# Optimization experiments

Measured on AMD Instinct MI355X. Metric: run time of the kernel, lower is better.

## Reference

```python
import jax, jax.numpy as jnp
import numpy as np

D = 768           # input_dim == slot_dim
H, DH = 8, 64     # encoder attention heads / head dim (x-transformers defaults)
INNER = 4 * D     # ff_mult=4 GLU inner dim
EPS = 1e-8
N_ITERS = 3
SCALE = D ** -0.5


def _ln(x, g, b):
    m = jnp.mean(x, axis=-1, keepdims=True)
    v = jnp.var(x, axis=-1, keepdims=True)
    return (x - m) / jnp.sqrt(v + 1e-5) * g + b


def setup_inputs() -> dict:
    key = jax.random.key(0)
    ks = jax.random.split(key, 16)
    w = lambda i, shape, s=0.02: jax.random.normal(ks[i], shape, jnp.float32) * s
    return dict(
        x=jax.random.normal(ks[0], (32, 1024, D), jnp.float32),
        noise=jax.random.normal(ks[1], (32, 16, D), jnp.float32),
        init_mu=jax.random.normal(ks[2], (D,), jnp.float32),
        init_log_sigma=w(3, (D,), 0.05),
        Wk=w(4, (D, D)), Wv=w(5, (D, D)), Wq=w(6, (D, D)),
        ni_g=jnp.ones(D), ni_b=jnp.zeros(D),       # norm_input
        ns_g=jnp.ones(D), ns_b=jnp.zeros(D),       # norm_slots
        nica_g=jnp.ones(D), nica_b=jnp.zeros(D),   # norm_ica
        ln1_g=jnp.ones(D), ln1_b=jnp.zeros(D),     # encoder attn pre-norm
        Wq_a=w(7, (D, H * DH)), Wk_a=w(8, (D, H * DH)),
        Wv_a=w(9, (D, H * DH)), Wo_a=w(10, (H * DH, D)),
        ln2_g=jnp.ones(D), ln2_b=jnp.zeros(D),     # encoder ff pre-norm
        W1=w(11, (D, 2 * INNER)), W2=w(12, (INNER, D)),
        lnf_g=jnp.ones(D), lnf_b=jnp.zeros(D),     # encoder final norm
    )


def _inv_cross_attn(q, k, v):
    # softmax over the SLOT axis (dim i), then renormalize over keys j
    dots = jnp.einsum('bid,bjd->bij', q, k) * SCALE
    attn = jax.nn.softmax(dots, axis=1) + EPS
    attn = attn / jnp.sum(attn, axis=-1, keepdims=True)
    updates = jnp.einsum('bjd,bij->bid', v, attn)
    return updates, attn


def _encoder(h, ln1_g, ln1_b, Wq_a, Wk_a, Wv_a, Wo_a, ln2_g, ln2_b, W1, W2, lnf_g, lnf_b):
    b, n, _ = h.shape
    a = _ln(h, ln1_g, ln1_b)
    q = (a @ Wq_a).reshape(b, n, H, DH)
    k = (a @ Wk_a).reshape(b, n, H, DH)
    v = (a @ Wv_a).reshape(b, n, H, DH)
    scores = jnp.einsum('bihd,bjhd->bhij', q, k) * (DH ** -0.5)
    p = jax.nn.softmax(scores, axis=-1)
    o = jnp.einsum('bhij,bjhd->bihd', p, v).reshape(b, n, H * DH)
    h = h + o @ Wo_a
    f = _ln(h, ln2_g, ln2_b)
    u, g = jnp.split(f @ W1, 2, axis=-1)
    h = h + (u * jax.nn.silu(g)) @ W2
    return _ln(h, lnf_g, lnf_b)


def reference(x, noise, init_mu, init_log_sigma, Wk, Wv, Wq,
              ni_g, ni_b, ns_g, ns_b, nica_g, nica_b,
              ln1_g, ln1_b, Wq_a, Wk_a, Wv_a, Wo_a,
              ln2_g, ln2_b, W1, W2, lnf_g, lnf_b):
    xn = _ln(x, ni_g, ni_b)
    k = xn @ Wk
    v = xn @ Wv
    slots = init_mu + jnp.exp(init_log_sigma) * noise  # [b, n_slots, d]

    def step(slots):
        q = _ln(slots, ns_g, ns_b) @ Wq
        updates, attn = _inv_cross_attn(q, k, v)
        slots = _ln(slots + updates, nica_g, nica_b)
        slots = _encoder(slots, ln1_g, ln1_b, Wq_a, Wk_a, Wv_a, Wo_a,
                         ln2_g, ln2_b, W1, W2, lnf_g, lnf_b)
        return slots, attn

    for _ in range(N_ITERS):
        slots, _ = step(slots)
    slots, attn = step(slots)
    attn_map = jnp.transpose(attn, (0, 2, 1))  # b n hw -> b hw n
    return slots, attn_map
```

## Files before the change

### kernel.cpp

```cpp
#include <hip/hip_runtime.h>
#include <hip/hip_bf16.h>
#include <stdint.h>

typedef _Float16 f16;
typedef __attribute__((ext_vector_type(8))) _Float16 f16x8;
typedef __attribute__((ext_vector_type(4))) _Float16 f16x4;
typedef __attribute__((ext_vector_type(4))) float f32x4;

#define GLOBAL_AS __attribute__((address_space(1)))
#define LDS_AS __attribute__((address_space(3)))

#define D_DIM 768
#define NTOK 1024
#define NSLOT 16
#define NB 32
#define NTOT (NB*NTOK)
#define HDIM 512
#define INNER 3072
#define SCALE_D 0.03608439182435161f
#define SCALE_H 0.125f

template<int OUT>
__global__ __launch_bounds__(256) void mgemm64_k(
    const f16* __restrict__ A, const f16* __restrict__ Bt,
    void* __restrict__ Cout, int M, int N, int K, int Kc)
{
  __shared__ __align__(16) f16 As[64*128];
  __shared__ __align__(16) f16 Bs[64*128];
  const int tid = threadIdx.x;
  const int lane = tid & 63;
  const int wave = tid >> 6;
  const int m0 = blockIdx.x*64, n0 = blockIdx.y*64;
  const int kbeg = blockIdx.z * Kc;
  const int wm = (wave>>1)*32, wn = (wave&1)*32;
  const int quad = lane>>4, l16 = lane&15;

  const int sr = tid>>2;
  const int sc = (tid&3)*8;
  const f16* gA = A  + (size_t)(m0+sr)*K + kbeg + sc;
  const f16* gB = Bt + (size_t)(n0+sr)*K + kbeg + sc;
  LDS_AS f16* lA = (LDS_AS f16*)&As[(size_t)tid*8];
  LDS_AS f16* lB = (LDS_AS f16*)&Bs[(size_t)tid*8];

  const f16* fA0 = &As[(wm + l16)*32 + quad*8];
  const f16* fB0 = &Bs[(wn + l16)*32 + quad*8];

  f32x4 acc[2][2] = {};

  for (int k0 = 0; k0 < Kc; k0 += 128){
    #pragma unroll
    for (int p=0;p<4;++p){
      __builtin_amdgcn_global_load_lds((const GLOBAL_AS void*)(gA + k0 + p*32),
                                       (LDS_AS void*)(lA + (size_t)p*2048), 16, 0, 0);
      __builtin_amdgcn_global_load_lds((const GLOBAL_AS void*)(gB + k0 + p*32),
                                       (LDS_AS void*)(lB + (size_t)p*2048), 16, 0, 0);
    }
    __syncthreads();
    #pragma unroll
    for (int p=0;p<4;++p){
      f16x8 a0 = *(const f16x8*)(fA0 + p*2048);
      f16x8 a1 = *(const f16x8*)(fA0 + p*2048 + 16*32);
      f16x8 b0 = *(const f16x8*)(fB0 + p*2048);
      f16x8 b1 = *(const f16x8*)(fB0 + p*2048 + 16*32);
      acc[0][0] = __builtin_amdgcn_mfma_f32_16x16x32_f16(a0,b0,acc[0][0],0,0,0);
      acc[0][1] = __builtin_amdgcn_mfma_f32_16x16x32_f16(a0,b1,acc[0][1],0,0,0);
      acc[1][0] = __builtin_amdgcn_mfma_f32_16x16x32_f16(a1,b0,acc[1][0],0,0,0);
      acc[1][1] = __builtin_amdgcn_mfma_f32_16x16x32_f16(a1,b1,acc[1][1],0,0,0);
    }
    __syncthreads();
  }
  #pragma unroll
  for (int mt=0;mt<2;++mt){
    #pragma unroll
    for (int nt=0;nt<2;++nt){
      int gm = m0 + wm + mt*16 + quad*4;
      int gn = n0 + wn + nt*16 + l16;
      #pragma unroll
      for (int r=0;r<4;++r){
        float c = acc[mt][nt][r];
        size_t idx = (size_t)(gm+r)*N + gn;
        if (OUT==1) ((f16*)Cout)[idx] = (f16)c;
        else        atomicAdd(&((float*)Cout)[idx], c);
      }
    }
  }
}

__global__ __launch_bounds__(256) void w1glu_k(
    const f16* __restrict__ A, const f16* __restrict__ W1T,
    f16* __restrict__ act, int M)
{
  __shared__ __align__(16) f16 As[64*128];
  __shared__ __align__(16) f16 Bu[64*128];
  __shared__ __align__(16) f16 Bg[64*128];
  const int K = 768;
  const int tid = threadIdx.x;
  const int lane = tid & 63;
  const int wave = tid >> 6;
  const int m0 = blockIdx.x*64, n0 = blockIdx.y*64;
  const int wm = (wave>>1)*32, wn = (wave&1)*32;
  const int quad = lane>>4, l16 = lane&15;

  const int sr = tid>>2;
  const int sc = (tid&3)*8;
  const f16* gA  = A   + (size_t)(m0+sr)*K + sc;
  const f16* gBu = W1T + (size_t)(n0+sr)*K + sc;
  const f16* gBg = W1T + (size_t)(3072+n0+sr)*K + sc;
  LDS_AS f16* lA  = (LDS_AS f16*)&As[(size_t)tid*8];
  LDS_AS f16* lBu = (LDS_AS f16*)&Bu[(size_t)tid*8];
  LDS_AS f16* lBg = (LDS_AS f16*)&Bg[(size_t)tid*8];

  const f16* fA0 = &As[(wm + l16)*32 + quad*8];
  const f16* fU0 = &Bu[(wn + l16)*32 + quad*8];
  const f16* fG0 = &Bg[(wn + l16)*32 + quad*8];

  f32x4 accU[2][2] = {};
  f32x4 accG[2][2] = {};

  for (int k0 = 0; k0 < K; k0 += 128){
    #pragma unroll
    for (int p=0;p<4;++p){
      __builtin_amdgcn_global_load_lds((const GLOBAL_AS void*)(gA  + k0 + p*32),
                                       (LDS_AS void*)(lA  + (size_t)p*2048), 16, 0, 0);
      __builtin_amdgcn_global_load_lds((const GLOBAL_AS void*)(gBu + k0 + p*32),
                                       (LDS_AS void*)(lBu + (size_t)p*2048), 16, 0, 0);
      __builtin_amdgcn_global_load_lds((const GLOBAL_AS void*)(gBg + k0 + p*32),
                                       (LDS_AS void*)(lBg + (size_t)p*2048), 16, 0, 0);
    }
    __syncthreads();
    #pragma unroll
    for (int p=0;p<4;++p){
      f16x8 a0 = *(const f16x8*)(fA0 + p*2048);
      f16x8 a1 = *(const f16x8*)(fA0 + p*2048 + 16*32);
      f16x8 u0 = *(const f16x8*)(fU0 + p*2048);
      f16x8 u1 = *(const f16x8*)(fU0 + p*2048 + 16*32);
      f16x8 g0 = *(const f16x8*)(fG0 + p*2048);
      f16x8 g1 = *(const f16x8*)(fG0 + p*2048 + 16*32);
      accU[0][0] = __builtin_amdgcn_mfma_f32_16x16x32_f16(a0,u0,accU[0][0],0,0,0);
      accU[0][1] = __builtin_amdgcn_mfma_f32_16x16x32_f16(a0,u1,accU[0][1],0,0,0);
      accU[1][0] = __builtin_amdgcn_mfma_f32_16x16x32_f16(a1,u0,accU[1][0],0,0,0);
      accU[1][1] = __builtin_amdgcn_mfma_f32_16x16x32_f16(a1,u1,accU[1][1],0,0,0);
      accG[0][0] = __builtin_amdgcn_mfma_f32_16x16x32_f16(a0,g0,accG[0][0],0,0,0);
      accG[0][1] = __builtin_amdgcn_mfma_f32_16x16x32_f16(a0,g1,accG[0][1],0,0,0);
      accG[1][0] = __builtin_amdgcn_mfma_f32_16x16x32_f16(a1,g0,accG[1][0],0,0,0);
      accG[1][1] = __builtin_amdgcn_mfma_f32_16x16x32_f16(a1,g1,accG[1][1],0,0,0);
    }
    __syncthreads();
  }
  #pragma unroll
  for (int mt=0;mt<2;++mt){
    #pragma unroll
    for (int nt=0;nt<2;++nt){
      int gm = m0 + wm + mt*16 + quad*4;
      int gn = n0 + wn + nt*16 + l16;
      #pragma unroll
      for (int r=0;r<4;++r){
        float u = accU[mt][nt][r];
        float g = accG[mt][nt][r];
        float sg = g / (1.0f + __expf(-g));
        act[(size_t)(gm+r)*INNER + gn] = (f16)(u*sg);
      }
    }
  }
}

__global__ __launch_bounds__(256) void dots_k(
    const f16* __restrict__ Q,
    const f16* __restrict__ Xn,
    f16* __restrict__ attn,
    float* __restrict__ rsPart)
{
  __shared__ __align__(16) f16 qf[16*768];
  __shared__ __align__(16) f16 ks[64*128];
  __shared__ float rpart[4][16];
  const int b = blockIdx.x, jt = blockIdx.y;
  const int tid = threadIdx.x;
  const int lane = tid & 63;
  const int w = tid >> 6;
  const int quad = lane>>4, l16 = lane&15;

  #pragma unroll
  for (int c=0;c<6;++c){
    int p = c*256 + tid;
    int ki = p >> 6, qd = (p >> 4) & 3, rw = p & 15;
    f16x8 v = *(const f16x8*)(Q + ((size_t)(b*NSLOT+rw))*D_DIM + ki*32 + qd*8);
    *(f16x8*)&qf[(size_t)p*8] = v;
  }

  const f16* gK = Xn + ((size_t)(b*NTOK + jt*64 + (tid>>2)))*D_DIM + (tid&3)*8;
  LDS_AS f16* lK = (LDS_AS f16*)&ks[(size_t)tid*8];

  f32x4 acc = {};
  for (int it=0; it<6; ++it){
    #pragma unroll
    for (int p=0;p<4;++p)
      __builtin_amdgcn_global_load_lds((const GLOBAL_AS void*)(gK + it*128 + p*32),
                                       (LDS_AS void*)(lK + (size_t)p*2048), 16, 0, 0);
    __syncthreads();
    #pragma unroll
    for (int p=0;p<4;++p){
      f16x8 a  = *(const f16x8*)&qf[(((size_t)(it*4+p)*4 + quad)*16 + l16)*8];
      f16x8 bf = *(const f16x8*)&ks[(size_t)p*2048 + (w*16+l16)*32 + quad*8];
      acc = __builtin_amdgcn_mfma_f32_16x16x32_f16(a, bf, acc, 0, 0, 0);
    }
    __syncthreads();
  }

  float v0 = acc[0]*SCALE_D, v1 = acc[1]*SCALE_D, v2 = acc[2]*SCALE_D, v3 = acc[3]*SCALE_D;
  float mx = fmaxf(fmaxf(v0,v1), fmaxf(v2,v3));
  mx = fmaxf(mx, __shfl_xor(mx, 16));
  mx = fmaxf(mx, __shfl_xor(mx, 32));
  float e0 = __expf(v0-mx), e1 = __expf(v1-mx), e2 = __expf(v2-mx), e3 = __expf(v3-mx);
  float s = e0+e1+e2+e3;
  s += __shfl_xor(s, 16);
  s += __shfl_xor(s, 32);
  float inv = 1.0f/s;
  float a0 = e0*inv + 1e-8f, a1 = e1*inv + 1e-8f, a2 = e2*inv + 1e-8f, a3 = e3*inv + 1e-8f;

  int jcol = jt*64 + w*16 + l16;
  int ibase = b*NSLOT + quad*4;
  attn[(size_t)(ibase+0)*NTOK + jcol] = (f16)a0;
  attn[(size_t)(ibase+1)*NTOK + jcol] = (f16)a1;
  attn[(size_t)(ibase+2)*NTOK + jcol] = (f16)a2;
  attn[(size_t)(ibase+3)*NTOK + jcol] = (f16)a3;

  float t0=a0, t1=a1, t2=a2, t3=a3;
  #pragma unroll
  for (int m=1;m<16;m<<=1){
    t0 += __shfl_xor(t0, m);
    t1 += __shfl_xor(t1, m);
    t2 += __shfl_xor(t2, m);
    t3 += __shfl_xor(t3, m);
  }
  if (l16 == 0){
    rpart[w][quad*4+0] = t0;
    rpart[w][quad*4+1] = t1;
    rpart[w][quad*4+2] = t2;
    rpart[w][quad*4+3] = t3;
  }
  __syncthreads();
  if (tid < 16){
    float ss = rpart[0][tid] + rpart[1][tid] + rpart[2][tid] + rpart[3][tid];
    rsPart[(size_t)((b*16 + jt)<<4) + tid] = ss;
  }
}

__global__ __launch_bounds__(256) void attnv_k(
    const f16* __restrict__ attn,
    const float* __restrict__ rsPart,
    const f16* __restrict__ XnT,
    const f16* __restrict__ WvT,
    float* __restrict__ accb)
{
  __shared__ __align__(16) f16 Asl[16*128];
  __shared__ __align__(16) f16 Bsl[64*128];
  __shared__ float rsum[16];
  __shared__ __align__(16) f16 tl[16][80];
  const int b = blockIdx.x, d0 = blockIdx.y*64;
  const int tid = threadIdx.x;
  const int lane = tid & 63;
  const int w = tid >> 6;
  const int quad = lane>>4, l16 = lane&15;

  if (tid < 16){
    float s = 0.f;
    #pragma unroll
    for (int jt=0;jt<16;++jt) s += rsPart[(size_t)((b*16 + jt)<<4) + tid];
    rsum[tid] = s;
  }

  const int pa = tid>>6, ta = tid&63;
  const f16* gA = attn + ((size_t)(b*NSLOT + (ta>>2)))*NTOK + pa*32 + (ta&3)*8;
  LDS_AS f16* lA = (LDS_AS f16*)&Asl[(size_t)pa*512 + ta*8];
  const f16* gB = XnT + ((size_t)(d0 + (tid>>2)))*NTOT + b*NTOK + (tid&3)*8;
  LDS_AS f16* lB = (LDS_AS f16*)&Bsl[(size_t)tid*8];

  f32x4 acc = {};
  for (int it=0; it<8; ++it){
    __builtin_amdgcn_global_load_lds((const GLOBAL_AS void*)(gA + it*128),
                                     (LDS_AS void*)lA, 16, 0, 0);
    #pragma unroll
    for (int p=0;p<4;++p)
      __builtin_amdgcn_global_load_lds((const GLOBAL_AS void*)(gB + it*128 + p*32),
                                       (LDS_AS void*)(lB + (size_t)p*2048), 16, 0, 0);
    __syncthreads();
    #pragma unroll
    for (int p=0;p<4;++p){
      f16x8 a  = *(const f16x8*)&Asl[(size_t)p*512 + l16*32 + quad*8];
      f16x8 bf = *(const f16x8*)&Bsl[(size_t)p*2048 + (w*16+l16)*32 + quad*8];
      acc = __builtin_amdgcn_mfma_f32_16x16x32_f16(a, bf, acc, 0, 0, 0);
    }
    __syncthreads();
  }
  const int dloc = w*16 + l16;
  #pragma unroll
  for (int r=0;r<4;++r)
    tl[quad*4+r][dloc] = (f16)(acc[r] / rsum[quad*4+r]);
  __syncthreads();
  f16x8 af0 = *(const f16x8*)&tl[l16][quad*8];
  f16x8 af1 = *(const f16x8*)&tl[l16][32 + quad*8];
  const f16* bp = WvT + (size_t)l16*D_DIM + d0 + quad*8;
  float* up = accb + (size_t)(b*NSLOT + quad*4)*D_DIM + l16;
  #pragma unroll
  for (int j=0;j<12;++j){
    int n0 = (w*12 + j)*16;
    f16x8 b0 = *(const f16x8*)(bp + (size_t)n0*D_DIM);
    f16x8 b1 = *(const f16x8*)(bp + (size_t)n0*D_DIM + 32);
    f32x4 c = {};
    c = __builtin_amdgcn_mfma_f32_16x16x32_f16(af0, b0, c, 0,0,0);
    c = __builtin_amdgcn_mfma_f32_16x16x32_f16(af1, b1, c, 0,0,0);
    #pragma unroll
    for (int r=0;r<4;++r) atomicAdd(up + (size_t)r*D_DIM + n0, c[r]);
  }
}

__global__ __launch_bounds__(256) void lnw_k(
    const float* __restrict__ X,
    const float* __restrict__ g, const float* __restrict__ bb,
    f16* __restrict__ out)
{
  const int lane = threadIdx.x & 63;
  const size_t row = (size_t)blockIdx.x*4 + (threadIdx.x>>6);
  const float* x = X + row*D_DIM;
  float4 v[3]; float s=0.f, ss=0.f;
  #pragma unroll
  for (int t=0;t<3;++t){
    v[t] = *(const float4*)(x + lane*4 + t*256);
    s  += v[t].x+v[t].y+v[t].z+v[t].w;
    ss += v[t].x*v[t].x+v[t].y*v[t].y+v[t].z*v[t].z+v[t].w*v[t].w;
  }
  #pragma unroll
  for (int m=1;m<64;m<<=1){ s += __shfl_xor(s,m); ss += __shfl_xor(ss,m); }
  float mean = s*(1.0f/768.0f);
  float inv  = rsqrtf(ss*(1.0f/768.0f) - mean*mean + 1e-5f);
  #pragma unroll
  for (int t=0;t<3;++t){
    int c0 = lane*4 + t*256;
    float4 gg = *(const float4*)(g + c0);
    float4 bv = *(const float4*)(bb + c0);
    f16x4 h4;
    h4.x = (f16)((v[t].x-mean)*inv*gg.x + bv.x);
    h4.y = (f16)((v[t].y-mean)*inv*gg.y + bv.y);
    h4.z = (f16)((v[t].z-mean)*inv*gg.z + bv.z);
    h4.w = (f16)((v[t].w-mean)*inv*gg.w + bv.w);
    *(f16x4*)(out + row*D_DIM + c0) = h4;
  }
}

template<bool WACC>
__global__ __launch_bounds__(256) void lnlnw_k(
    const float* __restrict__ X,
    const float* __restrict__ g1, const float* __restrict__ b1,
    const float* __restrict__ g2, const float* __restrict__ b2,
    float* __restrict__ out1, f16* __restrict__ out2, float* __restrict__ acc)
{
  const int lane = threadIdx.x & 63;
  const size_t row = (size_t)blockIdx.x*4 + (threadIdx.x>>6);
  const float* x = X + row*D_DIM;
  float4 v[3]; float s=0.f, ss=0.f;
  #pragma unroll
  for (int t=0;t<3;++t){
    v[t] = *(const float4*)(x + lane*4 + t*256);
    s  += v[t].x+v[t].y+v[t].z+v[t].w;
    ss += v[t].x*v[t].x+v[t].y*v[t].y+v[t].z*v[t].z+v[t].w*v[t].w;
  }
  #pragma unroll
  for (int m=1;m<64;m<<=1){ s += __shfl_xor(s,m); ss += __shfl_xor(ss,m); }
  float mean = s*(1.0f/768.0f);
  float inv  = rsqrtf(ss*(1.0f/768.0f) - mean*mean + 1e-5f);
  float y[3][4]; float s2=0.f, ss2=0.f;
  #pragma unroll
  for (int t=0;t<3;++t){
    int c0 = lane*4 + t*256;
    float4 gg = *(const float4*)(g1 + c0);
    float4 bv = *(const float4*)(b1 + c0);
    y[t][0] = (v[t].x-mean)*inv*gg.x + bv.x;
    y[t][1] = (v[t].y-mean)*inv*gg.y + bv.y;
    y[t][2] = (v[t].z-mean)*inv*gg.z + bv.z;
    y[t][3] = (v[t].w-mean)*inv*gg.w + bv.w;
    float4 o = { y[t][0], y[t][1], y[t][2], y[t][3] };
    *(float4*)(out1 + row*D_DIM + c0) = o;
    if (WACC) *(float4*)(acc + row*D_DIM + c0) = o;
    s2  += y[t][0]+y[t][1]+y[t][2]+y[t][3];
    ss2 += y[t][0]*y[t][0]+y[t][1]*y[t][1]+y[t][2]*y[t][2]+y[t][3]*y[t][3];
  }
  #pragma unroll
  for (int m=1;m<64;m<<=1){ s2 += __shfl_xor(s2,m); ss2 += __shfl_xor(ss2,m); }
  float mean2 = s2*(1.0f/768.0f);
  float inv2  = rsqrtf(ss2*(1.0f/768.0f) - mean2*mean2 + 1e-5f);
  #pragma unroll
  for (int t=0;t<3;++t){
    int c0 = lane*4 + t*256;
    float4 gg = *(const float4*)(g2 + c0);
    float4 bv = *(const float4*)(b2 + c0);
    f16x4 h4;
    h4.x = (f16)((y[t][0]-mean2)*inv2*gg.x + bv.x);
    h4.y = (f16)((y[t][1]-mean2)*inv2*gg.y + bv.y);
    h4.z = (f16)((y[t][2]-mean2)*inv2*gg.z + bv.z);
    h4.w = (f16)((y[t][3]-mean2)*inv2*gg.w + bv.w);
    *(f16x4*)(out2 + row*D_DIM + c0) = h4;
  }
}

__global__ __launch_bounds__(256) void slotsinit_k(
    const float* __restrict__ noise, const float* __restrict__ mu,
    const float* __restrict__ ls,
    const float* __restrict__ nsg, const float* __restrict__ nsb,
    float* __restrict__ slots, float* __restrict__ accb, f16* __restrict__ tmp2)
{
  const int lane = threadIdx.x & 63;
  const size_t row = (size_t)blockIdx.x*4 + (threadIdx.x>>6);
  float4 v[3]; float s=0.f, ss=0.f;
  #pragma unroll
  for (int t=0;t<3;++t){
    int c0 = lane*4 + t*256;
    float4 nz = *(const float4*)(noise + row*D_DIM + c0);
    float4 m4 = *(const float4*)(mu + c0);
    float4 l4 = *(const float4*)(ls + c0);
    v[t].x = m4.x + __expf(l4.x)*nz.x;
    v[t].y = m4.y + __expf(l4.y)*nz.y;
    v[t].z = m4.z + __expf(l4.z)*nz.z;
    v[t].w = m4.w + __expf(l4.w)*nz.w;
    *(float4*)(slots + row*D_DIM + c0) = v[t];
    *(float4*)(accb  + row*D_DIM + c0) = v[t];
    s  += v[t].x+v[t].y+v[t].z+v[t].w;
    ss += v[t].x*v[t].x+v[t].y*v[t].y+v[t].z*v[t].z+v[t].w*v[t].w;
  }
  #pragma unroll
  for (int m=1;m<64;m<<=1){ s += __shfl_xor(s,m); ss += __shfl_xor(ss,m); }
  float mean = s*(1.0f/768.0f);
  float inv  = rsqrtf(ss*(1.0f/768.0f) - mean*mean + 1e-5f);
  #pragma unroll
  for (int t=0;t<3;++t){
    int c0 = lane*4 + t*256;
    float4 gg = *(const float4*)(nsg + c0);
    float4 bv = *(const float4*)(nsb + c0);
    f16x4 h4;
    h4.x = (f16)((v[t].x-mean)*inv*gg.x + bv.x);
    h4.y = (f16)((v[t].y-mean)*inv*gg.y + bv.y);
    h4.z = (f16)((v[t].z-mean)*inv*gg.z + bv.z);
    h4.w = (f16)((v[t].w-mean)*inv*gg.w + bv.w);
    *(f16x4*)(tmp2 + row*D_DIM + c0) = h4;
  }
}

__global__ __launch_bounds__(256) void encwo_k(
    const f16* __restrict__ QA, const f16* __restrict__ KA,
    const f16* __restrict__ VA, int QSTR,
    const f16* __restrict__ WoT,
    float* __restrict__ hb)
{
  __shared__ float qs[16][68], ks[16][68], vs[16][68], ps[16][20];
  __shared__ __align__(16) f16 ol[16][80];
  const int b = blockIdx.x, h = blockIdx.y;
  const int tid = threadIdx.x;
  {
    int i = tid>>4, dd=(tid&15)*4;
    size_t base = ((size_t)(b*NSLOT+i))*QSTR + h*64 + dd;
    f16x4 uq = *(const f16x4*)(QA + base);
    f16x4 uk = *(const f16x4*)(KA + base);
    f16x4 uv = *(const f16x4*)(VA + base);
    float4 fq = { (float)uq.x, (float)uq.y, (float)uq.z, (float)uq.w };
    float4 fk = { (float)uk.x, (float)uk.y, (float)uk.z, (float)uk.w };
    float4 fv = { (float)uv.x, (float)uv.y, (float)uv.z, (float)uv.w };
    *(float4*)&qs[i][dd]=fq; *(float4*)&ks[i][dd]=fk; *(float4*)&vs[i][dd]=fv;
  }
  __syncthreads();
  {
    int i = tid>>4, j = tid&15;
    float s=0.f;
    #pragma unroll 8
    for (int d=0; d<64; ++d) s += qs[i][d]*ks[j][d];
    ps[i][j] = s*SCALE_H;
  }
  __syncthreads();
  if (tid < 16){
    int i = tid;
    float mx=-1e30f;
    #pragma unroll
    for (int j=0;j<16;++j) mx = fmaxf(mx, ps[i][j]);
    float sm=0.f;
    #pragma unroll
    for (int j=0;j<16;++j){ float e=__expf(ps[i][j]-mx); ps[i][j]=e; sm+=e; }
    float inv=1.0f/sm;
    #pragma unroll
    for (int j=0;j<16;++j) ps[i][j]*=inv;
  }
  __syncthreads();
  {
    int i = tid>>4, dq=(tid&15)*4;
    float a0=0,a1=0,a2=0,a3=0;
    #pragma unroll
    for (int j=0;j<16;++j){
      float p = ps[i][j];
      a0+=p*vs[j][dq+0]; a1+=p*vs[j][dq+1]; a2+=p*vs[j][dq+2]; a3+=p*vs[j][dq+3];
    }
    f16x4 o4 = { (f16)a0, (f16)a1, (f16)a2, (f16)a3 };
    *(f16x4*)&ol[i][dq] = o4;
  }
  __syncthreads();
  const int lane = tid & 63, w = tid>>6, quad = lane>>4, l16 = lane&15;
  f16x8 af0 = *(const f16x8*)&ol[l16][quad*8];
  f16x8 af1 = *(const f16x8*)&ol[l16][32 + quad*8];
  const f16* bp = WoT + (size_t)l16*HDIM + h*64 + quad*8;
  float* hp = hb + (size_t)(b*NSLOT + quad*4)*D_DIM + l16;
  #pragma unroll
  for (int j=0;j<12;++j){
    int n0 = (w*12 + j)*16;
    f16x8 b0 = *(const f16x8*)(bp + (size_t)n0*HDIM);
    f16x8 b1 = *(const f16x8*)(bp + (size_t)n0*HDIM + 32);
    f32x4 c = {};
    c = __builtin_amdgcn_mfma_f32_16x16x32_f16(af0, b0, c, 0,0,0);
    c = __builtin_amdgcn_mfma_f32_16x16x32_f16(af1, b1, c, 0,0,0);
    #pragma unroll
    for (int r=0;r<4;++r) atomicAdd(hp + (size_t)r*D_DIM + n0, c[r]);
  }
}

__global__ __launch_bounds__(256) void transp_k(
    const f16* __restrict__ in, f16* __restrict__ out, int R, int C)
{
  __shared__ f16 T[64][72];
  const int m0 = blockIdx.x*64, d0 = blockIdx.y*64;
  const int tid = threadIdx.x;
  {
    int r = tid>>2, c = (tid&3)*16;
    const f16* p = in + (size_t)(m0+r)*C + d0 + c;
    *(f16x8*)&T[r][c]   = *(const f16x8*)p;
    *(f16x8*)&T[r][c+8] = *(const f16x8*)(p+8);
  }
  __syncthreads();
  {
    int dd = tid>>2, mq = (tid&3)*16;
    f16 v[16];
    #pragma unroll
    for (int e=0;e<16;++e) v[e] = T[mq+e][dd];
    f16* p = out + (size_t)(d0+dd)*R + m0 + mq;
    *(f16x8*)p     = *(f16x8*)&v[0];
    *(f16x8*)(p+8) = *(f16x8*)&v[8];
  }
}

__global__ __launch_bounds__(256) void prep_k(
    const float* __restrict__ Wv,   const float* __restrict__ Wq_a,
    const float* __restrict__ Wk_a, const float* __restrict__ Wv_a,
    const float* __restrict__ Wo_a, const float* __restrict__ W1,
    const float* __restrict__ W2,   const float* __restrict__ Wk,
    const float* __restrict__ Wq,
    f16* __restrict__ WvT, f16* __restrict__ WqkvT, f16* __restrict__ WoaT,
    f16* __restrict__ W1T, f16* __restrict__ W2T,
    f16* __restrict__ Wkf, f16* __restrict__ Wqf)
{
  __shared__ float t[32][33];
  int bid = blockIdx.x;
  const float* src; f16* dst; int R, C; bool tr = true;
  if      (bid < 576)  {              src=Wv;   dst=WvT;             R=768;  C=768; }
  else if (bid < 960)  { bid-=576;    src=Wq_a; dst=WqkvT;           R=768;  C=512; }
  else if (bid < 1344) { bid-=960;    src=Wk_a; dst=WqkvT+512*768;   R=768;  C=512; }
  else if (bid < 1728) { bid-=1344;   src=Wv_a; dst=WqkvT+1024*768;  R=768;  C=512; }
  else if (bid < 2112) { bid-=1728;   src=Wo_a; dst=WoaT;            R=512;  C=768; }
  else if (bid < 6720) { bid-=2112;   src=W1;   dst=W1T;             R=768;  C=6144; }
  else if (bid < 9024) { bid-=6720;   src=W2;   dst=W2T;             R=3072; C=768; }
  else if (bid < 9600) { bid-=9024;   src=Wk;   dst=Wkf;             R=768;  C=768; tr=false; }
  else                 { bid-=9600;   src=Wq;   dst=Wqf;             R=768;  C=768; tr=false; }
  const int tpr = C/32;
  const int r0 = (bid / tpr)*32, c0 = (bid % tpr)*32;
  const int lc = threadIdx.x & 31, g8 = threadIdx.x >> 5;
  if (tr){
    #pragma unroll
    for (int s=0;s<4;++s){
      int r = g8*4 + s;
      t[r][lc] = src[(size_t)(r0+r)*C + c0+lc];
    }
    __syncthreads();
    #pragma unroll
    for (int s=0;s<4;++s){
      int c = g8*4 + s;
      dst[(size_t)(c0+c)*R + r0+lc] = (f16)t[lc][c];
    }
  } else {
    #pragma unroll
    for (int s=0;s<4;++s){
      int r = g8*4 + s;
      dst[(size_t)(r0+r)*C + c0+lc] = (f16)src[(size_t)(r0+r)*C + c0+lc];
    }
  }
}

__global__ __launch_bounds__(256) void attnout_k(
    const f16* __restrict__ attn, const float* __restrict__ rsPart,
    float* __restrict__ out)
{
  __shared__ float rsum[16];
  const int bid = blockIdx.x, tid = threadIdx.x;
  const int b = bid >> 6;
  if (tid < 16){
    float s = 0.f;
    #pragma unroll
    for (int jt=0;jt<16;++jt) s += rsPart[(size_t)((b*16+jt)<<4) + tid];
    rsum[tid] = s;
  }
  __syncthreads();
  int idx = bid*256 + tid;
  int i = idx & 15;
  int j = (idx >> 4) & 1023;
  out[idx] = (float)attn[((size_t)(b*NSLOT)+i)*NTOK + j] / rsum[i];
}

extern "C" void kernel_launch(void* const* d_in, const int* in_sizes, int n_in,
                              void* d_out, int out_size, void* d_ws, size_t ws_size,
                              hipStream_t stream) {
  const float* x        = (const float*)d_in[0];
  const float* noise    = (const float*)d_in[1];
  const float* init_mu  = (const float*)d_in[2];
  const float* init_ls  = (const float*)d_in[3];
  const float* Wk       = (const float*)d_in[4];
  const float* Wv       = (const float*)d_in[5];
  const float* Wq       = (const float*)d_in[6];
  const float* ni_g     = (const float*)d_in[7];
  const float* ni_b     = (const float*)d_in[8];
  const float* ns_g     = (const float*)d_in[9];
  const float* ns_b     = (const float*)d_in[10];
  const float* nica_g   = (const float*)d_in[11];
  const float* nica_b   = (const float*)d_in[12];
  const float* ln1_g    = (const float*)d_in[13];
  const float* ln1_b    = (const float*)d_in[14];
  const float* Wq_a     = (const float*)d_in[15];
  const float* Wk_a     = (const float*)d_in[16];
  const float* Wv_a     = (const float*)d_in[17];
  const float* Wo_a     = (const float*)d_in[18];
  const float* ln2_g    = (const float*)d_in[19];
  const float* ln2_b    = (const float*)d_in[20];
  const float* W1       = (const float*)d_in[21];
  const float* W2       = (const float*)d_in[22];
  const float* lnf_g    = (const float*)d_in[23];
  const float* lnf_b    = (const float*)d_in[24];

  char* w = (char*)d_ws;
  size_t off = 0;
  auto alloc = [&](size_t bytes)->char*{
    char* p = w + off; off += (bytes + 255) & ~(size_t)255; return p;
  };
  f16* xn_h  = (f16*)alloc((size_t)NTOT*D_DIM*2);
  f16* xnT_h = (f16*)alloc((size_t)D_DIM*NTOT*2);
  f16* Wkf   = (f16*)alloc((size_t)768*768*2);
  f16* Wqf   = (f16*)alloc((size_t)768*768*2);
  f16* BtQK  = (f16*)alloc((size_t)768*768*2);
  f16* WvT   = (f16*)alloc((size_t)768*768*2);
  f16* WqkvT = (f16*)alloc((size_t)1536*768*2);
  f16* WoaT  = (f16*)alloc((size_t)768*512*2);
  f16* W1T   = (f16*)alloc((size_t)6144*768*2);
  f16* W2T   = (f16*)alloc((size_t)768*3072*2);
  float* slots = (float*)alloc(512*768*4);
  float* hbuf  = (float*)alloc(512*768*4);
  float* accb  = (float*)alloc(512*768*4);
  f16* tmp_h  = (f16*)alloc(512*768*2);
  f16* tmp2_h = (f16*)alloc(512*768*2);
  f16* q_h    = (f16*)alloc(512*768*2);
  f16* qkv_h  = (f16*)alloc((size_t)512*1536*2);
  f16* act_h  = (f16*)alloc((size_t)512*3072*2);
  f16* attn_h = (f16*)alloc((size_t)NB*NSLOT*NTOK*2);
  float* rsPart = (float*)alloc((size_t)32*16*16*4);

  prep_k<<<10176, 256, 0, stream>>>(Wv, Wq_a, Wk_a, Wv_a, Wo_a, W1, W2, Wk, Wq,
                                    WvT, WqkvT, WoaT, W1T, W2T, Wkf, Wqf);

  mgemm64_k<1><<<dim3(12, 12, 1), 256, 0, stream>>>(Wkf, Wqf, BtQK, 768, 768, 768, 768);

  lnw_k<<<NTOT/4, 256, 0, stream>>>(x, ni_g, ni_b, xn_h);
  transp_k<<<dim3(NTOT/64, D_DIM/64), 256, 0, stream>>>(xn_h, xnT_h, NTOT, D_DIM);

  slotsinit_k<<<128, 256, 0, stream>>>(noise, init_mu, init_ls, ns_g, ns_b,
                                       slots, accb, tmp2_h);

  for (int it=0; it<4; ++it){
    mgemm64_k<1><<<dim3(8, 12, 1), 256, 0, stream>>>(tmp2_h, BtQK, q_h, 512, 768, 768, 768);
    dots_k<<<dim3(NB, 16), 256, 0, stream>>>(q_h, xn_h, attn_h, rsPart);
    attnv_k<<<dim3(NB, 12), 256, 0, stream>>>(attn_h, rsPart, xnT_h, WvT, accb);
    lnlnw_k<false><<<128, 256, 0, stream>>>(accb, nica_g, nica_b, ln1_g, ln1_b,
                                            hbuf, tmp_h, nullptr);
    mgemm64_k<1><<<dim3(8, 24, 1), 256, 0, stream>>>(tmp_h, WqkvT, qkv_h, 512, 1536, 768, 768);
    encwo_k<<<dim3(NB, 8), 256, 0, stream>>>(qkv_h, qkv_h + 512, qkv_h + 1024, 1536,
                                             WoaT, hbuf);
    lnw_k<<<128, 256, 0, stream>>>(hbuf, ln2_g, ln2_b, tmp_h);
    w1glu_k<<<dim3(8, 48), 256, 0, stream>>>(tmp_h, W1T, act_h, 512);
    mgemm64_k<2><<<dim3(8, 12, 4), 256, 0, stream>>>(act_h, W2T, hbuf, 512, 768, 3072, 768);
    lnlnw_k<true><<<128, 256, 0, stream>>>(hbuf, lnf_g, lnf_b, ns_g, ns_b,
                                           slots, tmp2_h, accb);
  }

  hipMemcpyAsync(d_out, slots, (size_t)512*768*4, hipMemcpyDeviceToDevice, stream);
  attnout_k<<<NB*NTOK*NSLOT/256, 256, 0, stream>>>(attn_h, rsPart, (float*)d_out + 512*768);
}
```

Measured before the change: 713.3 us.

## Double-buffer GEMM staging and replace atomic epilogues with separate plain-store GEMMs

Adds two-stage LDS double buffering with explicit waitcnt/barrier scheduling to the generic GEMM, GLU GEMM, dots and attn·V kernels, so the next K tile loads while the current one is computed. Removes the fused Wv and Wo projections that used float atomics, running them as separate GEMMs with plain stores. The W2 GEMM is no longer split-K with atomics, and residual adds move into the layernorm kernels. This trades atomic traffic and memset-style accumulation for extra launches, doubled LDS use (lower occupancy), and less parallelism in the W2 GEMM.

```diff
diff --git a/kernel.cpp b/kernel.cpp
--- a/kernel.cpp
+++ b/kernel.cpp
@@ -23,39 +23,51 @@
 template<int OUT>
 __global__ __launch_bounds__(256) void mgemm64_k(
     const f16* __restrict__ A, const f16* __restrict__ Bt,
-    void* __restrict__ Cout, int M, int N, int K, int Kc)
-{
-  __shared__ __align__(16) f16 As[64*128];
-  __shared__ __align__(16) f16 Bs[64*128];
+    void* __restrict__ Cout, int M, int N, int K, int nsteps)
+{
+  __shared__ __align__(16) f16 As[2][64*128];
+  __shared__ __align__(16) f16 Bs[2][64*128];
   const int tid = threadIdx.x;
   const int lane = tid & 63;
   const int wave = tid >> 6;
   const int m0 = blockIdx.x*64, n0 = blockIdx.y*64;
-  const int kbeg = blockIdx.z * Kc;
   const int wm = (wave>>1)*32, wn = (wave&1)*32;
   const int quad = lane>>4, l16 = lane&15;
 
   const int sr = tid>>2;
   const int sc = (tid&3)*8;
-  const f16* gA = A  + (size_t)(m0+sr)*K + kbeg + sc;
-  const f16* gB = Bt + (size_t)(n0+sr)*K + kbeg + sc;
-  LDS_AS f16* lA = (LDS_AS f16*)&As[(size_t)tid*8];
-  LDS_AS f16* lB = (LDS_AS f16*)&Bs[(size_t)tid*8];
-
-  const f16* fA0 = &As[(wm + l16)*32 + quad*8];
-  const f16* fB0 = &Bs[(wn + l16)*32 + quad*8];
+  const f16* gA = A  + (size_t)(m0+sr)*K + sc;
+  const f16* gB = Bt + (size_t)(n0+sr)*K + sc;
 
   f32x4 acc[2][2] = {};
 
-  for (int k0 = 0; k0 < Kc; k0 += 128){
+  auto stage = [&](int t, int buf){
+    LDS_AS f16* lA = (LDS_AS f16*)&As[buf][(size_t)tid*8];
+    LDS_AS f16* lB = (LDS_AS f16*)&Bs[buf][(size_t)tid*8];
+    const f16* pA = gA + t*128;
+    const f16* pB = gB + t*128;
     #pragma unroll
     for (int p=0;p<4;++p){
-      __builtin_amdgcn_global_load_lds((const GLOBAL_AS void*)(gA + k0 + p*32),
+      __builtin_amdgcn_global_load_lds((const GLOBAL_AS void*)(pA + p*32),
                                        (LDS_AS void*)(lA + (size_t)p*2048), 16, 0, 0);
-      __builtin_amdgcn_global_load_lds((const GLOBAL_AS void*)(gB + k0 + p*32),
+      __builtin_amdgcn_global_load_lds((const GLOBAL_AS void*)(pB + p*32),
                                        (LDS_AS void*)(lB + (size_t)p*2048), 16, 0, 0);
     }
-    __syncthreads();
+  };
+
+  stage(0, 0);
+  for (int t=0; t<nsteps; ++t){
+    const int cur = t & 1;
+    if (t+1 < nsteps){
+      stage(t+1, cur^1);
+      asm volatile("s_waitcnt vmcnt(8) lgkmcnt(0)" ::: "memory");
+    } else {
+      asm volatile("s_waitcnt vmcnt(0) lgkmcnt(0)" ::: "memory");
+    }
+    __builtin_amdgcn_s_barrier();
+    __builtin_amdgcn_sched_barrier(0);
+    const f16* fA0 = &As[cur][(wm + l16)*32 + quad*8];
+    const f16* fB0 = &Bs[cur][(wn + l16)*32 + quad*8];
     #pragma unroll
     for (int p=0;p<4;++p){
       f16x8 a0 = *(const f16x8*)(fA0 + p*2048);
@@ -67,7 +79,8 @@
       acc[1][0] = __builtin_amdgcn_mfma_f32_16x16x32_f16(a1,b0,acc[1][0],0,0,0);
       acc[1][1] = __builtin_amdgcn_mfma_f32_16x16x32_f16(a1,b1,acc[1][1],0,0,0);
     }
-    __syncthreads();
+    __builtin_amdgcn_sched_barrier(0);
+    __builtin_amdgcn_s_barrier();
   }
   #pragma unroll
   for (int mt=0;mt<2;++mt){
@@ -80,7 +93,7 @@
         float c = acc[mt][nt][r];
         size_t idx = (size_t)(gm+r)*N + gn;
         if (OUT==1) ((f16*)Cout)[idx] = (f16)c;
-        else        atomicAdd(&((float*)Cout)[idx], c);
+        else        ((float*)Cout)[idx] = c;
       }
     }
   }
@@ -90,9 +103,9 @@
     const f16* __restrict__ A, const f16* __restrict__ W1T,
     f16* __restrict__ act, int M)
 {
-  __shared__ __align__(16) f16 As[64*128];
-  __shared__ __align__(16) f16 Bu[64*128];
-  __shared__ __align__(16) f16 Bg[64*128];
+  __shared__ __align__(16) f16 As[2][64*128];
+  __shared__ __align__(16) f16 Bu[2][64*128];
+  __shared__ __align__(16) f16 Bg[2][64*128];
   const int K = 768;
   const int tid = threadIdx.x;
   const int lane = tid & 63;
@@ -106,28 +119,39 @@
   const f16* gA  = A   + (size_t)(m0+sr)*K + sc;
   const f16* gBu = W1T + (size_t)(n0+sr)*K + sc;
   const f16* gBg = W1T + (size_t)(3072+n0+sr)*K + sc;
-  LDS_AS f16* lA  = (LDS_AS f16*)&As[(size_t)tid*8];
-  LDS_AS f16* lBu = (LDS_AS f16*)&Bu[(size_t)tid*8];
-  LDS_AS f16* lBg = (LDS_AS f16*)&Bg[(size_t)tid*8];
-
-  const f16* fA0 = &As[(wm + l16)*32 + quad*8];
-  const f16* fU0 = &Bu[(wn + l16)*32 + quad*8];
-  const f16* fG0 = &Bg[(wn + l16)*32 + quad*8];
 
   f32x4 accU[2][2] = {};
   f32x4 accG[2][2] = {};
 
-  for (int k0 = 0; k0 < K; k0 += 128){
+  auto stage = [&](int t, int buf){
+    LDS_AS f16* lA  = (LDS_AS f16*)&As[buf][(size_t)tid*8];
+    LDS_AS f16* lBu = (LDS_AS f16*)&Bu[buf][(size_t)tid*8];
+    LDS_AS f16* lBg = (LDS_AS f16*)&Bg[buf][(size_t)tid*8];
     #pragma unroll
     for (int p=0;p<4;++p){
-      __builtin_amdgcn_global_load_lds((const GLOBAL_AS void*)(gA  + k0 + p*32),
+      __builtin_amdgcn_global_load_lds((const GLOBAL_AS void*)(gA  + t*128 + p*32),
                                        (LDS_AS void*)(lA  + (size_t)p*2048), 16, 0, 0);
-      __builtin_amdgcn_global_load_lds((const GLOBAL_AS void*)(gBu + k0 + p*32),
+      __builtin_amdgcn_global_load_lds((const GLOBAL_AS void*)(gBu + t*128 + p*32),
                                        (LDS_AS void*)(lBu + (size_t)p*2048), 16, 0, 0);
-      __builtin_amdgcn_global_load_lds((const GLOBAL_AS void*)(gBg + k0 + p*32),
+      __builtin_amdgcn_global_load_lds((const GLOBAL_AS void*)(gBg + t*128 + p*32),
                                        (LDS_AS void*)(lBg + (size_t)p*2048), 16, 0, 0);
     }
-    __syncthreads();
+  };
+
+  stage(0, 0);
+  for (int t=0; t<6; ++t){
+    const int cur = t & 1;
+    if (t+1 < 6){
+      stage(t+1, cur^1);
+      asm volatile("s_waitcnt vmcnt(12) lgkmcnt(0)" ::: "memory");
+    } else {
+      asm volatile("s_waitcnt vmcnt(0) lgkmcnt(0)" ::: "memory");
+    }
+    __builtin_amdgcn_s_barrier();
+    __builtin_amdgcn_sched_barrier(0);
+    const f16* fA0 = &As[cur][(wm + l16)*32 + quad*8];
+    const f16* fU0 = &Bu[cur][(wn + l16)*32 + quad*8];
+    const f16* fG0 = &Bg[cur][(wn + l16)*32 + quad*8];
     #pragma unroll
     for (int p=0;p<4;++p){
       f16x8 a0 = *(const f16x8*)(fA0 + p*2048);
@@ -145,7 +169,8 @@
       accG[1][0] = __builtin_amdgcn_mfma_f32_16x16x32_f16(a1,g0,accG[1][0],0,0,0);
       accG[1][1] = __builtin_amdgcn_mfma_f32_16x16x32_f16(a1,g1,accG[1][1],0,0,0);
     }
-    __syncthreads();
+    __builtin_amdgcn_sched_barrier(0);
+    __builtin_amdgcn_s_barrier();
   }
   #pragma unroll
   for (int mt=0;mt<2;++mt){
@@ -171,7 +196,7 @@
     float* __restrict__ rsPart)
 {
   __shared__ __align__(16) f16 qf[16*768];
-  __shared__ __align__(16) f16 ks[64*128];
+  __shared__ __align__(16) f16 ks[2][64*128];
   __shared__ float rpart[4][16];
   const int b = blockIdx.x, jt = blockIdx.y;
   const int tid = threadIdx.x;
@@ -188,22 +213,36 @@
   }
 
   const f16* gK = Xn + ((size_t)(b*NTOK + jt*64 + (tid>>2)))*D_DIM + (tid&3)*8;
-  LDS_AS f16* lK = (LDS_AS f16*)&ks[(size_t)tid*8];
+  auto stage = [&](int t, int buf){
+    LDS_AS f16* lK = (LDS_AS f16*)&ks[buf][(size_t)tid*8];
+    #pragma unroll
+    for (int p=0;p<4;++p)
+      __builtin_amdgcn_global_load_lds((const GLOBAL_AS void*)(gK + t*128 + p*32),
+                                       (LDS_AS void*)(lK + (size_t)p*2048), 16, 0, 0);
+  };
+
+  stage(0, 0);
+  __syncthreads();
 
   f32x4 acc = {};
   for (int it=0; it<6; ++it){
-    #pragma unroll
-    for (int p=0;p<4;++p)
-      __builtin_amdgcn_global_load_lds((const GLOBAL_AS void*)(gK + it*128 + p*32),
-                                       (LDS_AS void*)(lK + (size_t)p*2048), 16, 0, 0);
-    __syncthreads();
+    const int cur = it & 1;
+    if (it+1 < 6){
+      stage(it+1, cur^1);
+      asm volatile("s_waitcnt vmcnt(4) lgkmcnt(0)" ::: "memory");
+    } else {
+      asm volatile("s_waitcnt vmcnt(0) lgkmcnt(0)" ::: "memory");
+    }
+    __builtin_amdgcn_s_barrier();
+    __builtin_amdgcn_sched_barrier(0);
     #pragma unroll
     for (int p=0;p<4;++p){
       f16x8 a  = *(const f16x8*)&qf[(((size_t)(it*4+p)*4 + quad)*16 + l16)*8];
-      f16x8 bf = *(const f16x8*)&ks[(size_t)p*2048 + (w*16+l16)*32 + quad*8];
+      f16x8 bf = *(const f16x8*)&ks[cur][(size_t)p*2048 + (w*16+l16)*32 + quad*8];
       acc = __builtin_amdgcn_mfma_f32_16x16x32_f16(a, bf, acc, 0, 0, 0);
     }
-    __syncthreads();
+    __builtin_amdgcn_sched_barrier(0);
+    __builtin_amdgcn_s_barrier();
   }
 
   float v0 = acc[0]*SCALE_D, v1 = acc[1]*SCALE_D, v2 = acc[2]*SCALE_D, v3 = acc[3]*SCALE_D;
@@ -249,13 +288,11 @@
     const f16* __restrict__ attn,
     const float* __restrict__ rsPart,
     const f16* __restrict__ XnT,
-    const f16* __restrict__ WvT,
-    float* __restrict__ accb)
-{
-  __shared__ __align__(16) f16 Asl[16*128];
-  __shared__ __align__(16) f16 Bsl[64*128];
+    f16* __restrict__ t_out)
+{
+  __shared__ __align__(16) f16 Asl[2][16*128];
+  __shared__ __align__(16) f16 Bsl[2][64*128];
   __shared__ float rsum[16];
-  __shared__ __align__(16) f16 tl[16][80];
   const int b = blockIdx.x, d0 = blockIdx.y*64;
   const int tid = threadIdx.x;
   const int lane = tid & 63;
@@ -271,46 +308,45 @@
 
   const int pa = tid>>6, ta = tid&63;
   const f16* gA = attn + ((size_t)(b*NSLOT + (ta>>2)))*NTOK + pa*32 + (ta&3)*8;
-  LDS_AS f16* lA = (LDS_AS f16*)&Asl[(size_t)pa*512 + ta*8];
   const f16* gB = XnT + ((size_t)(d0 + (tid>>2)))*NTOT + b*NTOK + (tid&3)*8;
-  LDS_AS f16* lB = (LDS_AS f16*)&Bsl[(size_t)tid*8];
-
+
+  auto stage = [&](int t, int buf){
+    LDS_AS f16* lA = (LDS_AS f16*)&Asl[buf][(size_t)pa*512 + ta*8];
+    LDS_AS f16* lB = (LDS_AS f16*)&Bsl[buf][(size_t)tid*8];
+    __builtin_amdgcn_global_load_lds((const GLOBAL_AS void*)(gA + t*128),
+                                     (LDS_AS void*)lA, 16, 0, 0);
+    #pragma unroll
+    for (int p=0;p<4;++p)
+      __builtin_amdgcn_global_load_lds((const GLOBAL_AS void*)(gB + t*128 + p*32),
+                                       (LDS_AS void*)(lB + (size_t)p*2048), 16, 0, 0);
+  };
+
+  stage(0, 0);
   f32x4 acc = {};
   for (int it=0; it<8; ++it){
-    __builtin_amdgcn_global_load_lds((const GLOBAL_AS void*)(gA + it*128),
-                                     (LDS_AS void*)lA, 16, 0, 0);
-    #pragma unroll
-    for (int p=0;p<4;++p)
-      __builtin_amdgcn_global_load_lds((const GLOBAL_AS void*)(gB + it*128 + p*32),
-                                       (LDS_AS void*)(lB + (size_t)p*2048), 16, 0, 0);
-    __syncthreads();
+    const int cur = it & 1;
+    if (it+1 < 8){
+      stage(it+1, cur^1);
+      asm volatile("s_waitcnt vmcnt(5) lgkmcnt(0)" ::: "memory");
+    } else {
+      asm volatile("s_waitcnt vmcnt(0) lgkmcnt(0)" ::: "memory");
+    }
+    __builtin_amdgcn_s_barrier();
+    __builtin_amdgcn_sched_barrier(0);
     #pragma unroll
     for (int p=0;p<4;++p){
-      f16x8 a  = *(const f16x8*)&Asl[(size_t)p*512 + l16*32 + quad*8];
-      f16x8 bf = *(const f16x8*)&Bsl[(size_t)p*2048 + (w*16+l16)*32 + quad*8];
+      f16x8 a  = *(const f16x8*)&Asl[cur][(size_t)p*512 + l16*32 + quad*8];
+      f16x8 bf = *(const f16x8*)&Bsl[cur][(size_t)p*2048 + (w*16+l16)*32 + quad*8];
       acc = __builtin_amdgcn_mfma_f32_16x16x32_f16(a, bf, acc, 0, 0, 0);
     }
-    __syncthreads();
-  }
-  const int dloc = w*16 + l16;
-  #pragma unroll
-  for (int r=0;r<4;++r)
-    tl[quad*4+r][dloc] = (f16)(acc[r] / rsum[quad*4+r]);
-  __syncthreads();
-  f16x8 af0 = *(const f16x8*)&tl[l16][quad*8];
-  f16x8 af1 = *(const f16x8*)&tl[l16][32 + quad*8];
-  const f16* bp = WvT + (size_t)l16*D_DIM + d0 + quad*8;
-  float* up = accb + (size_t)(b*NSLOT + quad*4)*D_DIM + l16;
-  #pragma unroll
-  for (int j=0;j<12;++j){
-    int n0 = (w*12 + j)*16;
-    f16x8 b0 = *(const f16x8*)(bp + (size_t)n0*D_DIM);
-    f16x8 b1 = *(const f16x8*)(bp + (size_t)n0*D_DIM + 32);
-    f32x4 c = {};
-    c = __builtin_amdgcn_mfma_f32_16x16x32_f16(af0, b0, c, 0,0,0);
-    c = __builtin_amdgcn_mfma_f32_16x16x32_f16(af1, b1, c, 0,0,0);
-    #pragma unroll
-    for (int r=0;r<4;++r) atomicAdd(up + (size_t)r*D_DIM + n0, c[r]);
+    __builtin_amdgcn_sched_barrier(0);
+    __builtin_amdgcn_s_barrier();
+  }
+  int dcol = d0 + w*16 + l16;
+  #pragma unroll
+  for (int r=0;r<4;++r){
+    int i = quad*4 + r;
+    t_out[(size_t)(b*NSLOT + i)*D_DIM + dcol] = (f16)(acc[r] / rsum[i]);
   }
 }
 
@@ -347,20 +383,61 @@
   }
 }
 
-template<bool WACC>
+__global__ __launch_bounds__(256) void lnaddwb_k(
+    float* __restrict__ X, const float* __restrict__ X2,
+    const float* __restrict__ g, const float* __restrict__ bb,
+    f16* __restrict__ out)
+{
+  const int lane = threadIdx.x & 63;
+  const size_t row = (size_t)blockIdx.x*4 + (threadIdx.x>>6);
+  float* x = X + row*D_DIM;
+  const float* x2 = X2 + row*D_DIM;
+  float4 v[3]; float s=0.f, ss=0.f;
+  #pragma unroll
+  for (int t=0;t<3;++t){
+    int c0 = lane*4 + t*256;
+    float4 a = *(const float4*)(x + c0);
+    float4 b = *(const float4*)(x2 + c0);
+    v[t].x = a.x+b.x; v[t].y = a.y+b.y; v[t].z = a.z+b.z; v[t].w = a.w+b.w;
+    *(float4*)(x + c0) = v[t];
+    s  += v[t].x+v[t].y+v[t].z+v[t].w;
+    ss += v[t].x*v[t].x+v[t].y*v[t].y+v[t].z*v[t].z+v[t].w*v[t].w;
+  }
+  #pragma unroll
+  for (int m=1;m<64;m<<=1){ s += __shfl_xor(s,m); ss += __shfl_xor(ss,m); }
+  float mean = s*(1.0f/768.0f);
+  float inv  = rsqrtf(ss*(1.0f/768.0f) - mean*mean + 1e-5f);
+  #pragma unroll
+  for (int t=0;t<3;++t){
+    int c0 = lane*4 + t*256;
+    float4 gg = *(const float4*)(g + c0);
+    float4 bv = *(const float4*)(bb + c0);
+    f16x4 h4;
+    h4.x = (f16)((v[t].x-mean)*inv*gg.x + bv.x);
+    h4.y = (f16)((v[t].y-mean)*inv*gg.y + bv.y);
+    h4.z = (f16)((v[t].z-mean)*inv*gg.z + bv.z);
+    h4.w = (f16)((v[t].w-mean)*inv*gg.w + bv.w);
+    *(f16x4*)(out + row*D_DIM + c0) = h4;
+  }
+}
+
 __global__ __launch_bounds__(256) void lnlnw_k(
-    const float* __restrict__ X,
+    const float* __restrict__ X, const float* __restrict__ X2,
     const float* __restrict__ g1, const float* __restrict__ b1,
     const float* __restrict__ g2, const float* __restrict__ b2,
-    float* __restrict__ out1, f16* __restrict__ out2, float* __restrict__ acc)
+    float* __restrict__ out1, f16* __restrict__ out2)
 {
   const int lane = threadIdx.x & 63;
   const size_t row = (size_t)blockIdx.x*4 + (threadIdx.x>>6);
   const float* x = X + row*D_DIM;
+  const float* x2 = X2 + row*D_DIM;
   float4 v[3]; float s=0.f, ss=0.f;
   #pragma unroll
   for (int t=0;t<3;++t){
-    v[t] = *(const float4*)(x + lane*4 + t*256);
+    int c0 = lane*4 + t*256;
+    float4 a = *(const float4*)(x + c0);
+    float4 b = *(const float4*)(x2 + c0);
+    v[t].x = a.x+b.x; v[t].y = a.y+b.y; v[t].z = a.z+b.z; v[t].w = a.w+b.w;
     s  += v[t].x+v[t].y+v[t].z+v[t].w;
     ss += v[t].x*v[t].x+v[t].y*v[t].y+v[t].z*v[t].z+v[t].w*v[t].w;
   }
@@ -380,7 +457,6 @@
     y[t][3] = (v[t].w-mean)*inv*gg.w + bv.w;
     float4 o = { y[t][0], y[t][1], y[t][2], y[t][3] };
     *(float4*)(out1 + row*D_DIM + c0) = o;
-    if (WACC) *(float4*)(acc + row*D_DIM + c0) = o;
     s2  += y[t][0]+y[t][1]+y[t][2]+y[t][3];
     ss2 += y[t][0]*y[t][0]+y[t][1]*y[t][1]+y[t][2]*y[t][2]+y[t][3]*y[t][3];
   }
@@ -406,7 +482,7 @@
     const float* __restrict__ noise, const float* __restrict__ mu,
     const float* __restrict__ ls,
     const float* __restrict__ nsg, const float* __restrict__ nsb,
-    float* __restrict__ slots, float* __restrict__ accb, f16* __restrict__ tmp2)
+    float* __restrict__ slots, f16* __restrict__ tmp2)
 {
   const int lane = threadIdx.x & 63;
   const size_t row = (size_t)blockIdx.x*4 + (threadIdx.x>>6);
@@ -422,7 +498,6 @@
     v[t].z = m4.z + __expf(l4.z)*nz.z;
     v[t].w = m4.w + __expf(l4.w)*nz.w;
     *(float4*)(slots + row*D_DIM + c0) = v[t];
-    *(float4*)(accb  + row*D_DIM + c0) = v[t];
     s  += v[t].x+v[t].y+v[t].z+v[t].w;
     ss += v[t].x*v[t].x+v[t].y*v[t].y+v[t].z*v[t].z+v[t].w*v[t].w;
   }
@@ -444,14 +519,12 @@
   }
 }
 
-__global__ __launch_bounds__(256) void encwo_k(
+__global__ __launch_bounds__(256) void encattn_k(
     const f16* __restrict__ QA, const f16* __restrict__ KA,
     const f16* __restrict__ VA, int QSTR,
-    const f16* __restrict__ WoT,
-    float* __restrict__ hb)
+    f16* __restrict__ O)
 {
   __shared__ float qs[16][68], ks[16][68], vs[16][68], ps[16][20];
-  __shared__ __align__(16) f16 ol[16][80];
   const int b = blockIdx.x, h = blockIdx.y;
   const int tid = threadIdx.x;
   {
@@ -495,25 +568,8 @@
       float p = ps[i][j];
       a0+=p*vs[j][dq+0]; a1+=p*vs[j][dq+1]; a2+=p*vs[j][dq+2]; a3+=p*vs[j][dq+3];
     }
-    f16x4 o4 = { (f16)a0, (f16)a1, (f16)a2, (f16)a3 };
-    *(f16x4*)&ol[i][dq] = o4;
-  }
-  __syncthreads();
-  const int lane = tid & 63, w = tid>>6, quad = lane>>4, l16 = lane&15;
-  f16x8 af0 = *(const f16x8*)&ol[l16][quad*8];
-  f16x8 af1 = *(const f16x8*)&ol[l16][32 + quad*8];
-  const f16* bp = WoT + (size_t)l16*HDIM + h*64 + quad*8;
-  float* hp = hb + (size_t)(b*NSLOT + quad*4)*D_DIM + l16;
-  #pragma unroll
-  for (int j=0;j<12;++j){
-    int n0 = (w*12 + j)*16;
-    f16x8 b0 = *(const f16x8*)(bp + (size_t)n0*HDIM);
-    f16x8 b1 = *(const f16x8*)(bp + (size_t)n0*HDIM + 32);
-    f32x4 c = {};
-    c = __builtin_amdgcn_mfma_f32_16x16x32_f16(af0, b0, c, 0,0,0);
-    c = __builtin_amdgcn_mfma_f32_16x16x32_f16(af1, b1, c, 0,0,0);
-    #pragma unroll
-    for (int r=0;r<4;++r) atomicAdd(hp + (size_t)r*D_DIM + n0, c[r]);
+    size_t base = ((size_t)(b*NSLOT+i))*HDIM + h*64 + dq;
+    O[base+0]=(f16)a0; O[base+1]=(f16)a1; O[base+2]=(f16)a2; O[base+3]=(f16)a3;
   }
 }
 
@@ -653,11 +709,15 @@
   f16* W2T   = (f16*)alloc((size_t)768*3072*2);
   float* slots = (float*)alloc(512*768*4);
   float* hbuf  = (float*)alloc(512*768*4);
-  float* accb  = (float*)alloc(512*768*4);
+  float* upd   = (float*)alloc(512*768*4);
+  float* obuf  = (float*)alloc(512*768*4);
+  float* w2out = (float*)alloc(512*768*4);
   f16* tmp_h  = (f16*)alloc(512*768*2);
   f16* tmp2_h = (f16*)alloc(512*768*2);
   f16* q_h    = (f16*)alloc(512*768*2);
+  f16* t_h    = (f16*)alloc(512*768*2);
   f16* qkv_h  = (f16*)alloc((size_t)512*1536*2);
+  f16* o_h    = (f16*)alloc(512*512*2);
   f16* act_h  = (f16*)alloc((size_t)512*3072*2);
   f16* attn_h = (f16*)alloc((size_t)NB*NSLOT*NTOK*2);
   float* rsPart = (float*)alloc((size_t)32*16*16*4);
@@ -665,28 +725,29 @@
   prep_k<<<10176, 256, 0, stream>>>(Wv, Wq_a, Wk_a, Wv_a, Wo_a, W1, W2, Wk, Wq,
                                     WvT, WqkvT, WoaT, W1T, W2T, Wkf, Wqf);
 
-  mgemm64_k<1><<<dim3(12, 12, 1), 256, 0, stream>>>(Wkf, Wqf, BtQK, 768, 768, 768, 768);
+  mgemm64_k<1><<<dim3(12, 12), 256, 0, stream>>>(Wkf, Wqf, BtQK, 768, 768, 768, 6);
 
   lnw_k<<<NTOT/4, 256, 0, stream>>>(x, ni_g, ni_b, xn_h);
   transp_k<<<dim3(NTOT/64, D_DIM/64), 256, 0, stream>>>(xn_h, xnT_h, NTOT, D_DIM);
 
   slotsinit_k<<<128, 256, 0, stream>>>(noise, init_mu, init_ls, ns_g, ns_b,
-                                       slots, accb, tmp2_h);
+                                       slots, tmp2_h);
 
   for (int it=0; it<4; ++it){
-    mgemm64_k<1><<<dim3(8, 12, 1), 256, 0, stream>>>(tmp2_h, BtQK, q_h, 512, 768, 768, 768);
+    mgemm64_k<1><<<dim3(8, 12), 256, 0, stream>>>(tmp2_h, BtQK, q_h, 512, 768, 768, 6);
     dots_k<<<dim3(NB, 16), 256, 0, stream>>>(q_h, xn_h, attn_h, rsPart);
-    attnv_k<<<dim3(NB, 12), 256, 0, stream>>>(attn_h, rsPart, xnT_h, WvT, accb);
-    lnlnw_k<false><<<128, 256, 0, stream>>>(accb, nica_g, nica_b, ln1_g, ln1_b,
-                                            hbuf, tmp_h, nullptr);
-    mgemm64_k<1><<<dim3(8, 24, 1), 256, 0, stream>>>(tmp_h, WqkvT, qkv_h, 512, 1536, 768, 768);
-    encwo_k<<<dim3(NB, 8), 256, 0, stream>>>(qkv_h, qkv_h + 512, qkv_h + 1024, 1536,
-                                             WoaT, hbuf);
-    lnw_k<<<128, 256, 0, stream>>>(hbuf, ln2_g, ln2_b, tmp_h);
+    attnv_k<<<dim3(NB, 12), 256, 0, stream>>>(attn_h, rsPart, xnT_h, t_h);
+    mgemm64_k<0><<<dim3(8, 12), 256, 0, stream>>>(t_h, WvT, upd, 512, 768, 768, 6);
+    lnlnw_k<<<128, 256, 0, stream>>>(slots, upd, nica_g, nica_b, ln1_g, ln1_b,
+                                     hbuf, tmp_h);
+    mgemm64_k<1><<<dim3(8, 24), 256, 0, stream>>>(tmp_h, WqkvT, qkv_h, 512, 1536, 768, 6);
+    encattn_k<<<dim3(NB, 8), 256, 0, stream>>>(qkv_h, qkv_h + 512, qkv_h + 1024, 1536, o_h);
+    mgemm64_k<0><<<dim3(8, 12), 256, 0, stream>>>(o_h, WoaT, obuf, 512, 768, 512, 4);
+    lnaddwb_k<<<128, 256, 0, stream>>>(hbuf, obuf, ln2_g, ln2_b, tmp_h);
     w1glu_k<<<dim3(8, 48), 256, 0, stream>>>(tmp_h, W1T, act_h, 512);
-    mgemm64_k<2><<<dim3(8, 12, 4), 256, 0, stream>>>(act_h, W2T, hbuf, 512, 768, 3072, 768);
-    lnlnw_k<true><<<128, 256, 0, stream>>>(hbuf, lnf_g, lnf_b, ns_g, ns_b,
-                                           slots, tmp2_h, accb);
+    mgemm64_k<0><<<dim3(8, 12), 256, 0, stream>>>(act_h, W2T, w2out, 512, 768, 3072, 24);
+    lnlnw_k<<<128, 256, 0, stream>>>(hbuf, w2out, lnf_g, lnf_b, ns_g, ns_b,
+                                     slots, tmp2_h);
   }
 
   hipMemcpyAsync(d_out, slots, (size_t)512*768*4, hipMemcpyDeviceToDevice, stream);
```

Result: faster. 693.8 us (-2.7%).
